# Performance work log

Measured on AMD Instinct MI355X. Metric: run time of the kernel, lower is better.

Reference implementation:

```python
import jax, jax.numpy as jnp
import numpy as np
import math

D_MODEL = 1024
NUM_HEADS = 16
D_K = D_MODEL // NUM_HEADS
SEQ_LEN = 2048
THETA = 10000.0


def _rope_tables(seq_len, d_k, theta):
    # inv_freq over even dims, angles repeated-interleaved to full d_k
    inv_freq = theta ** (-jnp.arange(0, d_k, 2, dtype=jnp.float32) / d_k)  # [d_k/2]
    pos = jnp.arange(seq_len, dtype=jnp.float32)                          # [s]
    angles = pos[:, None] * inv_freq[None, :]                             # [s, d_k/2]
    angles = jnp.repeat(angles, 2, axis=-1)                               # [s, d_k]
    return jnp.cos(angles), jnp.sin(angles)


def _rotate_half(x):
    # interleaved pairs: (x0,x1,x2,x3,...) -> (-x1,x0,-x3,x2,...)
    x_even = x[..., ::2]
    x_odd = x[..., 1::2]
    return jnp.stack([-x_odd, x_even], axis=-1).reshape(x.shape)


def _apply_rope(x, cos, sin):
    # x: [b, h, s, d_k]; cos/sin: [s, d_k]
    return x * cos + _rotate_half(x) * sin


def setup_inputs() -> dict:
    key = jax.random.key(0)
    ks = jax.random.split(key, 5)
    scale = 1.0 / math.sqrt(D_MODEL)
    X = jax.random.normal(ks[0], (2, SEQ_LEN, D_MODEL), dtype=jnp.float32)
    Wq = jax.random.normal(ks[1], (D_MODEL, D_MODEL), dtype=jnp.float32) * scale
    Wk = jax.random.normal(ks[2], (D_MODEL, D_MODEL), dtype=jnp.float32) * scale
    Wv = jax.random.normal(ks[3], (D_MODEL, D_MODEL), dtype=jnp.float32) * scale
    Wo = jax.random.normal(ks[4], (D_MODEL, D_MODEL), dtype=jnp.float32) * scale
    return {"X": X, "Wq": Wq, "Wk": Wk, "Wv": Wv, "Wo": Wo}


def reference(X, Wq, Wk, Wv, Wo):
    b, s, _ = X.shape
    h, dk = NUM_HEADS, D_K

    def proj(W):
        return (X @ W.T).reshape(b, s, h, dk).transpose(0, 2, 1, 3)  # [b,h,s,dk]

    q, k, v = proj(Wq), proj(Wk), proj(Wv)

    cos, sin = _rope_tables(s, dk, THETA)
    q = _apply_rope(q, cos, sin)
    k = _apply_rope(k, cos, sin)

    scores = jnp.einsum('bhid,bhjd->bhij', q, k) / math.sqrt(dk)
    causal = jnp.tril(jnp.ones((s, s), dtype=bool))
    scores = jnp.where(causal[None, None], scores, -jnp.inf)
    probs = jax.nn.softmax(scores, axis=-1)
    attended = jnp.einsum('bhij,bhjd->bhid', probs, v)               # [b,h,s,dk]

    out = attended.transpose(0, 2, 1, 3).reshape(b, s, h * dk)
    return out @ Wo.T
```

## Files before the change

kernel.cpp:

```cpp
#include <hip/hip_runtime.h>
#include <stdint.h>

#define D_MODEL 1024
#define NUM_HEADS 16
#define DK 64
#define SEQ 2048
#define BATCH 2
#define MROWS (BATCH * SEQ)
#define LOG2E 1.4426950408889634f
#define FIXM 14.0f

typedef short bf16x8 __attribute__((ext_vector_type(8)));
typedef float f32x4 __attribute__((ext_vector_type(4)));
typedef float f32x16 __attribute__((ext_vector_type(16)));

__device__ __forceinline__ unsigned short f2bf(float f) {
    unsigned int u = __float_as_uint(f);
    u = (u + 0x7fffu + ((u >> 16) & 1u)) >> 16;
    return (unsigned short)u;
}
__device__ __forceinline__ float bf2f(unsigned short h) {
    return __uint_as_float(((unsigned int)h) << 16);
}
__device__ __forceinline__ void async16(const void* g, void* l) {
    __builtin_amdgcn_global_load_lds(
        (const __attribute__((address_space(1))) void*)g,
        (__attribute__((address_space(3))) void*)l, 16, 0, 0);
}
__device__ __forceinline__ unsigned int cvtpk(float lo, float hi) {
    unsigned int r;
    asm("v_cvt_pk_bf16_f32 %0, %1, %2" : "=v"(r) : "v"(lo), "v"(hi));
    return r;
}
#define SWZ64(row, b) ((((row) * 8) + ((b) ^ ((row) & 7))) * 8)

__global__ void cast_all(const float4* __restrict__ X, const float4* __restrict__ Wq,
                         const float4* __restrict__ Wk, const float4* __restrict__ Wv,
                         const float4* __restrict__ Wo, ushort4* __restrict__ Xb,
                         ushort4* __restrict__ Wqkvb, ushort4* __restrict__ Wob) {
    int i = blockIdx.x * blockDim.x + threadIdx.x;
    const float4* src;
    ushort4* dst;
    int off;
    if (i < 1048576) { src = X; dst = Xb; off = i; }
    else if (i < 1310720) { src = Wq; dst = Wqkvb; off = i - 1048576; }
    else if (i < 1572864) { src = Wk; dst = Wqkvb + 262144; off = i - 1310720; }
    else if (i < 1835008) { src = Wv; dst = Wqkvb + 524288; off = i - 1572864; }
    else { src = Wo; dst = Wob; off = i - 1835008; }
    float4 v = src[off];
    ushort4 o;
    o.x = f2bf(v.x); o.y = f2bf(v.y); o.z = f2bf(v.z); o.w = f2bf(v.w);
    dst[off] = o;
}

template <int TN, int OUT_BF16>
__global__ __launch_bounds__(256) void gemm_tile32(
    const unsigned short* __restrict__ A, const unsigned short* __restrict__ B,
    void* __restrict__ Cout, int M, int N, int K) {
    __shared__ unsigned short As[128 * 64];
    __shared__ unsigned short Bs[TN * 64];
    const int nwg = gridDim.x * gridDim.y;
    const int bid = blockIdx.y * gridDim.x + blockIdx.x;
    const int swz = (bid & 7) * (nwg >> 3) + (bid >> 3);
    const int m0 = (swz / gridDim.x) * 128, n0 = (swz % gridDim.x) * TN;
    const int t = threadIdx.x;
    const int lane = t & 63, wave = t >> 6;
    const int l31 = lane & 31, lh = lane >> 5;
    constexpr int MI = (TN == 128) ? 2 : 1;
    constexpr int NI = 2;
    const int wr = (TN == 128) ? (wave >> 1) * 64 : wave * 32;
    const int wc = (TN == 128) ? (wave & 1) * 64 : 0;

    f32x16 acc[MI][NI];
#pragma unroll
    for (int mi = 0; mi < MI; ++mi)
#pragma unroll
        for (int ni = 0; ni < NI; ++ni)
#pragma unroll
            for (int r = 0; r < 16; ++r) acc[mi][ni][r] = 0.f;

    for (int k0 = 0; k0 < K; k0 += 64) {
#pragma unroll
        for (int i = 0; i < 4; ++i) {
            int ch = i * 256 + t;
            int r = ch >> 3, b = (ch & 7) ^ (r & 7);
            async16(A + (size_t)(m0 + r) * K + k0 + b * 8, (char*)As + ch * 16);
        }
#pragma unroll
        for (int i = 0; i < TN / 32; ++i) {
            int ch = i * 256 + t;
            int r = ch >> 3, b = (ch & 7) ^ (r & 7);
            async16(B + (size_t)(n0 + r) * K + k0 + b * 8, (char*)Bs + ch * 16);
        }
        __syncthreads();
#pragma unroll
        for (int ks = 0; ks < 4; ++ks) {
            bf16x8 af[MI], bfr[NI];
#pragma unroll
            for (int mi = 0; mi < MI; ++mi)
                af[mi] = *(const bf16x8*)&As[SWZ64(wr + mi * 32 + l31, ks * 2 + lh)];
#pragma unroll
            for (int ni = 0; ni < NI; ++ni)
                bfr[ni] = *(const bf16x8*)&Bs[SWZ64(wc + ni * 32 + l31, ks * 2 + lh)];
#pragma unroll
            for (int mi = 0; mi < MI; ++mi)
#pragma unroll
                for (int ni = 0; ni < NI; ++ni)
                    acc[mi][ni] = __builtin_amdgcn_mfma_f32_32x32x16_bf16(
                        af[mi], bfr[ni], acc[mi][ni], 0, 0, 0);
        }
        __syncthreads();
    }
#pragma unroll
    for (int mi = 0; mi < MI; ++mi)
#pragma unroll
        for (int ni = 0; ni < NI; ++ni)
#pragma unroll
            for (int rg = 0; rg < 4; ++rg)
#pragma unroll
                for (int c = 0; c < 4; ++c) {
                    int gm = m0 + wr + mi * 32 + 8 * rg + 4 * lh + c;
                    int gn = n0 + wc + ni * 32 + l31;
                    float v = acc[mi][ni][rg * 4 + c];
                    if (OUT_BF16)
                        ((unsigned short*)Cout)[(size_t)gm * N + gn] = f2bf(v);
                    else
                        ((float*)Cout)[(size_t)gm * N + gn] = v;
                }
}

__global__ __launch_bounds__(256) void rope_vt(const unsigned short* __restrict__ QKV,
                                               unsigned short* __restrict__ Qr,
                                               unsigned short* __restrict__ Kr,
                                               unsigned short* __restrict__ Vt) {
    __shared__ unsigned short T[64][80];
    const int bx = blockIdx.x;
    const int t = threadIdx.x;
    if (bx < 4096) {
        int tid = bx * 256 + t;
        int bs = tid >> 8;
        int p4 = tid & 255;
        int b = bs >> 11, spos = bs & 2047;
        int h = p4 >> 4, dd = (p4 & 15) * 4;
        float sn0, cs0, sn1, cs1;
        {
            float if0 = __expf(-(float)dd * (9.210340371976184f / 64.0f));
            float if1 = __expf(-(float)(dd + 2) * (9.210340371976184f / 64.0f));
            __sincosf((float)spos * if0, &sn0, &cs0);
            __sincosf((float)spos * if1, &sn1, &cs1);
        }
        const float SCQ = 0.125f * LOG2E;
        float cs0q = cs0 * SCQ, sn0q = sn0 * SCQ;
        float cs1q = cs1 * SCQ, sn1q = sn1 * SCQ;
        size_t src = (size_t)bs * 3072 + h * 64 + dd;
        ushort4 qw = *(const ushort4*)&QKV[src];
        ushort4 kw = *(const ushort4*)&QKV[src + 1024];
        ushort4 qo_, ko_;
        float e = bf2f(qw.x), o = bf2f(qw.y);
        qo_.x = f2bf(e * cs0q - o * sn0q); qo_.y = f2bf(o * cs0q + e * sn0q);
        e = bf2f(qw.z); o = bf2f(qw.w);
        qo_.z = f2bf(e * cs1q - o * sn1q); qo_.w = f2bf(o * cs1q + e * sn1q);
        e = bf2f(kw.x); o = bf2f(kw.y);
        ko_.x = f2bf(e * cs0 - o * sn0); ko_.y = f2bf(o * cs0 + e * sn0);
        e = bf2f(kw.z); o = bf2f(kw.w);
        ko_.z = f2bf(e * cs1 - o * sn1); ko_.w = f2bf(o * cs1 + e * sn1);
        size_t qb = (((size_t)(b * NUM_HEADS + h) * SEQ + spos) * DK + dd);
        *(ushort4*)&Qr[qb] = qo_;
        *(ushort4*)&Kr[qb] = ko_;
    } else {
        int idx = bx - 4096;
        const int s0 = (idx & 31) * 64, bh = idx >> 5;
        const int b = bh >> 4, h = bh & 15;
#pragma unroll
        for (int i = 0; i < 2; ++i) {
            int ch = i * 256 + t;
            int row = ch >> 3, bc = ch & 7;
            *(int4*)&T[row][bc * 8] =
                *(const int4*)&QKV[(size_t)(b * SEQ + s0 + row) * 3072 + 2048 + h * 64 + bc * 8];
        }
        __syncthreads();
#pragma unroll
        for (int i = 0; i < 2; ++i) {
            int ch = i * 256 + t;
            int d = ch >> 3, sb = ch & 7;
            unsigned short tmp[8];
#pragma unroll
            for (int j = 0; j < 8; ++j) tmp[j] = T[sb * 8 + j][d];
            *(int4*)&Vt[(size_t)bh * DK * SEQ + (size_t)d * SEQ + s0 + sb * 8] = *(int4*)tmp;
        }
    }
}

__global__ __launch_bounds__(256, 5) void flash_attn10(
    const unsigned short* __restrict__ Qr, const unsigned short* __restrict__ Kr,
    const unsigned short* __restrict__ Vt, unsigned short* __restrict__ Att) {
    __shared__ unsigned short Ks[2][64 * 64];
    __shared__ unsigned short Vs[2][64 * 64];
    const int bh = blockIdx.x;
    const int qt = 31 - (int)blockIdx.y;
    const int t = threadIdx.x;
    const int lane = t & 63, wave = t >> 6;
    const int l31 = lane & 31, lh = lane >> 5;
    const int wq = wave >> 1, wd = wave & 1;
    const size_t qkbase = (size_t)bh * SEQ * DK;
    const unsigned short* Kg = Kr + qkbase;
    const unsigned short* Vg = Vt + (size_t)bh * DK * SEQ;
    const int qg = qt * 64 + wq * 32 + l31;

    bf16x8 aq[4];
#pragma unroll
    for (int kk = 0; kk < 4; ++kk)
        aq[kk] = *(const bf16x8*)&Qr[qkbase + (size_t)qg * DK + kk * 16 + lh * 8];

    f32x16 acc0, acc1;
#pragma unroll
    for (int r = 0; r < 16; ++r) { acc0[r] = 0.f; acc1[r] = 0.f; }
    float la[4] = {0.f, 0.f, 0.f, 0.f};

#pragma unroll
    for (int i = 0; i < 2; ++i) {
        int ch = i * 256 + t;
        int row = ch >> 3, sb = (ch & 7) ^ (row & 7);
        async16(Kg + (size_t)row * DK + sb * 8, (char*)Ks[0] + ch * 16);
        async16(Vg + (size_t)row * SEQ + sb * 8, (char*)Vs[0] + ch * 16);
    }

    for (int jt = 0; jt <= qt; ++jt) {
        __syncthreads();
        const int cur = jt & 1;
        if (jt < qt) {
            const int j1 = (jt + 1) * 64;
#pragma unroll
            for (int i = 0; i < 2; ++i) {
                int ch = i * 256 + t;
                int row = ch >> 3, sb = (ch & 7) ^ (row & 7);
                async16(Kg + (size_t)(j1 + row) * DK + sb * 8, (char*)Ks[cur ^ 1] + ch * 16);
                async16(Vg + (size_t)row * SEQ + j1 + sb * 8, (char*)Vs[cur ^ 1] + ch * 16);
            }
        }
        const unsigned short* Kt = Ks[cur];
        const unsigned short* Vtile = Vs[cur];
        const bool diag = (jt == qt);
        if (diag && wd > wq) continue;

        f32x16 s;
#pragma unroll
        for (int r = 0; r < 16; ++r) s[r] = 0.f;
        __builtin_amdgcn_s_setprio(1);
#pragma unroll
        for (int kk = 0; kk < 4; ++kk) {
            bf16x8 kf = *(const bf16x8*)&Kt[SWZ64(wd * 32 + l31, kk * 2 + lh)];
            s = __builtin_amdgcn_mfma_f32_32x32x16_bf16(kf, aq[kk], s, 0, 0, 0);
        }
        __builtin_amdgcn_s_setprio(0);
        if (diag && wd == wq) {
#pragma unroll
            for (int r = 0; r < 16; ++r) {
                int crow = (r & 3) + 8 * (r >> 2) + 4 * lh;
                if (crow > l31) s[r] = -1e30f;
            }
        }

#pragma unroll
        for (int r = 0; r < 16; ++r) {
            s[r] = __builtin_amdgcn_exp2f(s[r] - FIXM);
            la[r & 3] += s[r];
        }

        bf16x8 frA, frB;
        {
            unsigned int u0 = cvtpk(s[0], s[1]), v0 = cvtpk(s[4], s[5]);
            unsigned int u1 = cvtpk(s[2], s[3]), v1 = cvtpk(s[6], s[7]);
            asm("v_permlane32_swap_b32 %0, %1" : "+v"(u0), "+v"(v0));
            asm("v_permlane32_swap_b32 %0, %1" : "+v"(u1), "+v"(v1));
            uint4 w = {u0, u1, v0, v1};
            frA = *(bf16x8*)&w;
            unsigned int u2 = cvtpk(s[8], s[9]), v2 = cvtpk(s[12], s[13]);
            unsigned int u3 = cvtpk(s[10], s[11]), v3 = cvtpk(s[14], s[15]);
            asm("v_permlane32_swap_b32 %0, %1" : "+v"(u2), "+v"(v2));
            asm("v_permlane32_swap_b32 %0, %1" : "+v"(u3), "+v"(v3));
            uint4 w2_ = {u2, u3, v2, v3};
            frB = *(bf16x8*)&w2_;
        }

        __builtin_amdgcn_s_setprio(1);
        {
            bf16x8 vf0 = *(const bf16x8*)&Vtile[SWZ64(l31, (wd * 2 + 0) * 2 + lh)];
            bf16x8 vf2 = *(const bf16x8*)&Vtile[SWZ64(32 + l31, (wd * 2 + 0) * 2 + lh)];
            acc0 = __builtin_amdgcn_mfma_f32_32x32x16_bf16(vf0, frA, acc0, 0, 0, 0);
            acc1 = __builtin_amdgcn_mfma_f32_32x32x16_bf16(vf2, frA, acc1, 0, 0, 0);
            bf16x8 vf1 = *(const bf16x8*)&Vtile[SWZ64(l31, (wd * 2 + 1) * 2 + lh)];
            bf16x8 vf3 = *(const bf16x8*)&Vtile[SWZ64(32 + l31, (wd * 2 + 1) * 2 + lh)];
            acc0 = __builtin_amdgcn_mfma_f32_32x32x16_bf16(vf1, frB, acc0, 0, 0, 0);
            acc1 = __builtin_amdgcn_mfma_f32_32x32x16_bf16(vf3, frB, acc1, 0, 0, 0);
        }
        __builtin_amdgcn_s_setprio(0);
    }

    float lt = (la[0] + la[1]) + (la[2] + la[3]);
    lt += __shfl_xor(lt, 32, 64);
    __syncthreads();
    float* SC = (float*)Ks;
    float* LS = (float*)Vs;
    if (wd == 0) {
#pragma unroll
        for (int r = 0; r < 16; ++r) SC[(wq * 2 + 1) * 1024 + r * 64 + lane] = acc1[r];
    } else {
#pragma unroll
        for (int r = 0; r < 16; ++r) SC[(wq * 2 + 0) * 1024 + r * 64 + lane] = acc0[r];
    }
    if (lane < 32) LS[wave * 32 + l31] = lt;
    __syncthreads();
    const float rl = 1.0f / (LS[(wq * 2) * 32 + l31] + LS[(wq * 2 + 1) * 32 + l31]);
    float outv[16];
    if (wd == 0) {
#pragma unroll
        for (int r = 0; r < 16; ++r)
            outv[r] = acc0[r] + SC[(wq * 2 + 0) * 1024 + r * 64 + lane];
    } else {
#pragma unroll
        for (int r = 0; r < 16; ++r)
            outv[r] = acc1[r] + SC[(wq * 2 + 1) * 1024 + r * 64 + lane];
    }

    const int b_ = bh >> 4, h_ = bh & 15;
#pragma unroll
    for (int rg = 0; rg < 4; ++rg) {
        ushort4 o;
        o.x = f2bf(outv[rg * 4 + 0] * rl);
        o.y = f2bf(outv[rg * 4 + 1] * rl);
        o.z = f2bf(outv[rg * 4 + 2] * rl);
        o.w = f2bf(outv[rg * 4 + 3] * rl);
        *(ushort4*)&Att[(size_t)(b_ * SEQ + qg) * D_MODEL + h_ * DK + wd * 32 + 8 * rg + 4 * lh] = o;
    }
}

extern "C" void kernel_launch(void* const* d_in, const int* in_sizes, int n_in,
                              void* d_out, int out_size, void* d_ws, size_t ws_size,
                              hipStream_t stream) {
    const float* X = (const float*)d_in[0];
    const float* Wq = (const float*)d_in[1];
    const float* Wk = (const float*)d_in[2];
    const float* Wv = (const float*)d_in[3];
    const float* Wo = (const float*)d_in[4];

    char* ws = (char*)d_ws;
    unsigned short* Xb     = (unsigned short*)(ws + 0);
    unsigned short* Wqkvb  = (unsigned short*)(ws + (8u << 20));
    unsigned short* Wob    = (unsigned short*)(ws + (14u << 20));
    unsigned short* QKVraw = (unsigned short*)(ws + (16u << 20));
    unsigned short* Kr     = (unsigned short*)(ws + (40u << 20));
    unsigned short* Vt     = (unsigned short*)(ws + (48u << 20));
    unsigned short* Qr     = Xb;
    unsigned short* Att    = QKVraw;

    cast_all<<<8192, 256, 0, stream>>>((const float4*)X, (const float4*)Wq,
                                       (const float4*)Wk, (const float4*)Wv,
                                       (const float4*)Wo, (ushort4*)Xb,
                                       (ushort4*)Wqkvb, (ushort4*)Wob);

    gemm_tile32<128, 1><<<dim3(3072 / 128, MROWS / 128), 256, 0, stream>>>(
        Xb, Wqkvb, QKVraw, MROWS, 3072, D_MODEL);

    rope_vt<<<4096 + 1024, 256, 0, stream>>>(QKVraw, Qr, Kr, Vt);

    flash_attn10<<<dim3(BATCH * NUM_HEADS, 32), 256, 0, stream>>>(Qr, Kr, Vt, Att);

    gemm_tile32<64, 0><<<dim3(D_MODEL / 64, MROWS / 128), 256, 0, stream>>>(
        Att, Wob, d_out, MROWS, D_MODEL, D_MODEL);
}
```

Measured before the change: 182.6 us.

## Prefetch K two tiles ahead with triple buffer and explicit vmcnt waits

The flash attention kernel now keeps K tiles in a three-slot buffer and issues the K load two iterations ahead, while V stays double-buffered one tile ahead. The full __syncthreads is replaced by an explicit s_waitcnt vmcnt(2) plus s_barrier, so the in-flight K prefetch does not have to complete before the current tile is used. The PV MFMA order is also regrouped per accumulator. Shared memory grows from 32 KB to 40 KB and launch bounds drop from 5 to 4 blocks per CU, which lowers occupancy in exchange for deeper load latency hiding.

```diff
diff --git a/kernel.cpp b/kernel.cpp
--- a/kernel.cpp
+++ b/kernel.cpp
@@ -191,10 +191,10 @@
     }
 }
 
-__global__ __launch_bounds__(256, 5) void flash_attn10(
+__global__ __launch_bounds__(256, 4) void flash_attn13(
     const unsigned short* __restrict__ Qr, const unsigned short* __restrict__ Kr,
     const unsigned short* __restrict__ Vt, unsigned short* __restrict__ Att) {
-    __shared__ unsigned short Ks[2][64 * 64];
+    __shared__ unsigned short Ks3[3][64 * 64];
     __shared__ unsigned short Vs[2][64 * 64];
     const int bh = blockIdx.x;
     const int qt = 31 - (int)blockIdx.y;
@@ -221,25 +221,51 @@
     for (int i = 0; i < 2; ++i) {
         int ch = i * 256 + t;
         int row = ch >> 3, sb = (ch & 7) ^ (row & 7);
-        async16(Kg + (size_t)row * DK + sb * 8, (char*)Ks[0] + ch * 16);
+        async16(Kg + (size_t)row * DK + sb * 8, (char*)Ks3[0] + ch * 16);
+    }
+#pragma unroll
+    for (int i = 0; i < 2; ++i) {
+        int ch = i * 256 + t;
+        int row = ch >> 3, sb = (ch & 7) ^ (row & 7);
         async16(Vg + (size_t)row * SEQ + sb * 8, (char*)Vs[0] + ch * 16);
     }
+#pragma unroll
+    for (int i = 0; i < 2; ++i) {
+        int ch = i * 256 + t;
+        int row = ch >> 3, sb = (ch & 7) ^ (row & 7);
+        async16(Kg + (size_t)(64 + row) * DK + sb * 8, (char*)Ks3[1] + ch * 16);
+    }
 
     for (int jt = 0; jt <= qt; ++jt) {
-        __syncthreads();
-        const int cur = jt & 1;
-        if (jt < qt) {
+        if (jt < qt)
+            asm volatile("s_waitcnt vmcnt(2) lgkmcnt(0)" ::: "memory");
+        else
+            asm volatile("s_waitcnt vmcnt(0) lgkmcnt(0)" ::: "memory");
+        __builtin_amdgcn_s_barrier();
+        __builtin_amdgcn_sched_barrier(0);
+
+        if (jt + 1 <= qt) {
             const int j1 = (jt + 1) * 64;
 #pragma unroll
             for (int i = 0; i < 2; ++i) {
                 int ch = i * 256 + t;
                 int row = ch >> 3, sb = (ch & 7) ^ (row & 7);
-                async16(Kg + (size_t)(j1 + row) * DK + sb * 8, (char*)Ks[cur ^ 1] + ch * 16);
-                async16(Vg + (size_t)row * SEQ + j1 + sb * 8, (char*)Vs[cur ^ 1] + ch * 16);
+                async16(Vg + (size_t)row * SEQ + j1 + sb * 8,
+                        (char*)Vs[(jt + 1) & 1] + ch * 16);
             }
         }
-        const unsigned short* Kt = Ks[cur];
-        const unsigned short* Vtile = Vs[cur];
+        if (jt + 2 <= qt) {
+            const int j2 = (jt + 2) * 64;
+#pragma unroll
+            for (int i = 0; i < 2; ++i) {
+                int ch = i * 256 + t;
+                int row = ch >> 3, sb = (ch & 7) ^ (row & 7);
+                async16(Kg + (size_t)(j2 + row) * DK + sb * 8,
+                        (char*)Ks3[(jt + 2) % 3] + ch * 16);
+            }
+        }
+        const unsigned short* Kt = Ks3[jt % 3];
+        const unsigned short* Vtile = Vs[jt & 1];
         const bool diag = (jt == qt);
         if (diag && wd > wq) continue;
 
@@ -286,12 +312,12 @@
         __builtin_amdgcn_s_setprio(1);
         {
             bf16x8 vf0 = *(const bf16x8*)&Vtile[SWZ64(l31, (wd * 2 + 0) * 2 + lh)];
+            acc0 = __builtin_amdgcn_mfma_f32_32x32x16_bf16(vf0, frA, acc0, 0, 0, 0);
+            bf16x8 vf1 = *(const bf16x8*)&Vtile[SWZ64(l31, (wd * 2 + 1) * 2 + lh)];
+            acc0 = __builtin_amdgcn_mfma_f32_32x32x16_bf16(vf1, frB, acc0, 0, 0, 0);
             bf16x8 vf2 = *(const bf16x8*)&Vtile[SWZ64(32 + l31, (wd * 2 + 0) * 2 + lh)];
-            acc0 = __builtin_amdgcn_mfma_f32_32x32x16_bf16(vf0, frA, acc0, 0, 0, 0);
             acc1 = __builtin_amdgcn_mfma_f32_32x32x16_bf16(vf2, frA, acc1, 0, 0, 0);
-            bf16x8 vf1 = *(const bf16x8*)&Vtile[SWZ64(l31, (wd * 2 + 1) * 2 + lh)];
             bf16x8 vf3 = *(const bf16x8*)&Vtile[SWZ64(32 + l31, (wd * 2 + 1) * 2 + lh)];
-            acc0 = __builtin_amdgcn_mfma_f32_32x32x16_bf16(vf1, frB, acc0, 0, 0, 0);
             acc1 = __builtin_amdgcn_mfma_f32_32x32x16_bf16(vf3, frB, acc1, 0, 0, 0);
         }
         __builtin_amdgcn_s_setprio(0);
@@ -300,7 +326,7 @@
     float lt = (la[0] + la[1]) + (la[2] + la[3]);
     lt += __shfl_xor(lt, 32, 64);
     __syncthreads();
-    float* SC = (float*)Ks;
+    float* SC = (float*)Ks3;
     float* LS = (float*)Vs;
     if (wd == 0) {
 #pragma unroll
@@ -364,7 +390,7 @@
 
     rope_vt<<<4096 + 1024, 256, 0, stream>>>(QKVraw, Qr, Kr, Vt);
 
-    flash_attn10<<<dim3(BATCH * NUM_HEADS, 32), 256, 0, stream>>>(Qr, Kr, Vt, Att);
+    flash_attn13<<<dim3(BATCH * NUM_HEADS, 32), 256, 0, stream>>>(Qr, Kr, Vt, Att);
 
     gemm_tile32<64, 0><<<dim3(D_MODEL / 64, MROWS / 128), 256, 0, stream>>>(
         Att, Wob, d_out, MROWS, D_MODEL, D_MODEL);
```

New measurement: 169.6 us (median of 2 runs). 7.1% less time.
